# Kernel tuning notes

Measured on AMD Instinct MI355X. Metric: run time of the kernel, lower is better.

## Reference

```python
import jax, jax.numpy as jnp
import numpy as np

D_MODEL = 1024
OUTPUT_DIM = 1024
NUM_HEADS = 16
HEAD_DIM = D_MODEL // NUM_HEADS


def _xavier(key, shape):
    fan_in, fan_out = shape[1], shape[0]
    limit = float(np.sqrt(6.0 / (fan_in + fan_out)))
    return jax.random.uniform(key, shape, jnp.float32, -limit, limit)


def setup_inputs() -> dict:
    key = jax.random.key(0)
    k_h, k_q, k_k, k_o = jax.random.split(key, 4)
    H = jax.random.normal(k_h, (2, 2048, D_MODEL), dtype=jnp.float32)
    # nn.Linear weights are [out, in]; xavier_uniform on weights, default (uniform) biases left as zeros-equivalent
    Wq = _xavier(k_q, (D_MODEL, D_MODEL))
    bq = jnp.zeros((D_MODEL,), jnp.float32)
    Wk = _xavier(k_k, (D_MODEL, D_MODEL))
    bk = jnp.zeros((D_MODEL,), jnp.float32)
    Wo = _xavier(k_o, (OUTPUT_DIM, D_MODEL))
    bo = jnp.zeros((OUTPUT_DIM,), jnp.float32)
    return {"H": H, "Wq": Wq, "bq": bq, "Wk": Wk, "bk": bk, "Wo": Wo, "bo": bo}


def reference(H, Wq, bq, Wk, bk, Wo, bo):
    B, S, _ = H.shape
    Q = H @ Wq.T + bq  # [B,S,D]
    K = H @ Wk.T + bk
    # split heads -> [B,nh,S,hd]
    Qh = Q.reshape(B, S, NUM_HEADS, HEAD_DIM).transpose(0, 2, 1, 3)
    Kh = K.reshape(B, S, NUM_HEADS, HEAD_DIM).transpose(0, 2, 1, 3)
    Vh = H.reshape(B, S, NUM_HEADS, HEAD_DIM).transpose(0, 2, 1, 3)
    scale = 1.0 / jnp.sqrt(jnp.float32(HEAD_DIM))
    A = jnp.einsum('bhqd,bhkd->bhqk', Qh, Kh) * scale  # [B,nh,S,S]
    A = jax.nn.softmax(A, axis=-1)
    out = jnp.einsum('bhqk,bhkd->bhqd', A, Vh)  # [B,nh,S,hd]
    out = out.transpose(0, 2, 1, 3).reshape(B, S, D_MODEL)
    return out @ Wo.T + bo
```

## Files before the change

### kernel.cpp

```cpp
#include <hip/hip_runtime.h>
#include <stdint.h>

#define BB 2
#define SS 2048
#define DD 1024
#define NH 16
#define HD 64
#define MM 4096

typedef __bf16 bf16x8 __attribute__((ext_vector_type(8)));
typedef __bf16 bf16x4 __attribute__((ext_vector_type(4)));
typedef float  f32x4  __attribute__((ext_vector_type(4)));

__device__ __forceinline__ unsigned short f2bf(float f) {
    __bf16 h = (__bf16)f;
    return __builtin_bit_cast(unsigned short, h);
}

__device__ __forceinline__ void async_cp16(const void* g, const void* l) {
    __builtin_amdgcn_global_load_lds(
        (const __attribute__((address_space(1))) void*)(uintptr_t)g,
        (__attribute__((address_space(3))) void*)(uint32_t)(uintptr_t)l,
        16, 0, 0);
}

__device__ __forceinline__ f32x4 mfma16(bf16x8 a, bf16x8 b, f32x4 c) {
    return __builtin_amdgcn_mfma_f32_16x16x32_bf16(a, b, c, 0, 0, 0);
}

__global__ __launch_bounds__(256) void k_prep(const float* __restrict__ H,
                                              const float* __restrict__ Wq,
                                              const float* __restrict__ Wk,
                                              const float* __restrict__ Wo,
                                              unsigned short* __restrict__ Hb,
                                              unsigned short* __restrict__ Vt,
                                              unsigned short* __restrict__ Wqb,
                                              unsigned short* __restrict__ Wkb,
                                              unsigned short* __restrict__ Wob) {
    __shared__ float tile[128][68];
    const int bx = blockIdx.x;
    const int t = threadIdx.x;
    if (bx >= 512) {
        int g = bx - 512;
        const float* src; unsigned short* dst; int base;
        if (g < 512)       { src = Wq; dst = Wqb; base = g; }
        else if (g < 1024) { src = Wk; dst = Wkb; base = g - 512; }
        else               { src = Wo; dst = Wob; base = g - 1024; }
        int i = (base * 256 + t) * 8;
        float4 a = *(const float4*)(src + i);
        float4 b = *(const float4*)(src + i + 4);
        unsigned short o[8];
        o[0] = f2bf(a.x); o[1] = f2bf(a.y); o[2] = f2bf(a.z); o[3] = f2bf(a.w);
        o[4] = f2bf(b.x); o[5] = f2bf(b.y); o[6] = f2bf(b.z); o[7] = f2bf(b.w);
        *(ulonglong2*)(dst + i) = *(ulonglong2*)o;
        return;
    }
    const int sb = bx & 15, h = (bx >> 4) & 15, b = bx >> 8;
    const int col4 = t & 15;
    const int srow0 = t >> 4;
#pragma unroll
    for (int p = 0; p < 8; ++p) {
        int s = p * 16 + srow0;
        float4 v = *(const float4*)(H + (size_t)(b * SS + sb * 128 + s) * DD + h * HD + col4 * 4);
        *(float4*)&tile[s][col4 * 4] = v;
    }
    __syncthreads();
#pragma unroll
    for (int it = 0; it < 4; ++it) {
        int task = it * 256 + t;
        int s = task >> 3;
        int dg = task & 7;
        unsigned short pk[8];
#pragma unroll
        for (int j = 0; j < 8; ++j) pk[j] = f2bf(tile[s][dg * 8 + j]);
        *(ulonglong2*)(Hb + (size_t)(b * SS + sb * 128 + s) * DD + h * HD + dg * 8) = *(ulonglong2*)pk;
    }
#pragma unroll
    for (int it = 0; it < 4; ++it) {
        int task = it * 256 + t;
        int d = task >> 4;
        int sg = task & 15;
        unsigned short pk[8];
#pragma unroll
        for (int j = 0; j < 8; ++j) pk[j] = f2bf(tile[sg * 8 + j][d]);
        *(ulonglong2*)(Vt + (size_t)((b * NH + h) * HD + d) * SS + sb * 128 + sg * 8) = *(ulonglong2*)pk;
    }
}

template <int TM, bool BF16OUT>
__device__ __forceinline__ void gemm_body(const unsigned short* __restrict__ A,
                                          const unsigned short* __restrict__ Bt,
                                          const float* __restrict__ bias,
                                          void* __restrict__ Cp, float oscale) {
    constexpr int MT = TM / 32;
    constexpr int AR = TM / 32;
    __shared__ unsigned short lsA[2][TM * 64];
    __shared__ unsigned short lsB[2][128 * 64];
    const int tid = threadIdx.x;
    const int lane = tid & 63;
    const int w = tid >> 6;
    const int wm = w & 1, wn = w >> 1;
    const int r = lane & 15, quad = lane >> 4;
    const int mBase = blockIdx.y * TM;
    const int nBase = blockIdx.x * 128;

    const unsigned short* gA[AR]; uint laOff[AR];
#pragma unroll
    for (int t = 0; t < AR; ++t) {
        int l = t * 256 + tid;
        int c = l ^ ((l >> 3) & 7);
        int row = c >> 3, kc = c & 7;
        gA[t] = A + (size_t)(mBase + row) * 1024 + kc * 8;
        laOff[t] = l * 8;
    }
    const unsigned short* gB[4]; uint lbOff[4];
#pragma unroll
    for (int t = 0; t < 4; ++t) {
        int l = t * 256 + tid;
        int c = l ^ ((l >> 3) & 7);
        int row = c >> 3, kc = c & 7;
        gB[t] = Bt + (size_t)(nBase + row) * 1024 + kc * 8;
        lbOff[t] = l * 8;
    }
    uint aOff[2][MT], bOff[2][4];
#pragma unroll
    for (int hh = 0; hh < 2; ++hh) {
#pragma unroll
        for (int mt = 0; mt < MT; ++mt) {
            int rowA = wm * (TM / 2) + mt * 16 + r;
            int c = rowA * 8 + hh * 4 + quad;
            aOff[hh][mt] = (uint)((c ^ ((c >> 3) & 7)) * 8);
        }
#pragma unroll
        for (int nt = 0; nt < 4; ++nt) {
            int rowB = wn * 64 + nt * 16 + r;
            int c = rowB * 8 + hh * 4 + quad;
            bOff[hh][nt] = (uint)((c ^ ((c >> 3) & 7)) * 8);
        }
    }

    f32x4 acc[MT][4];
#pragma unroll
    for (int i = 0; i < MT; ++i)
#pragma unroll
        for (int j = 0; j < 4; ++j) acc[i][j] = f32x4{0.f, 0.f, 0.f, 0.f};

    auto stage = [&](int buf) {
#pragma unroll
        for (int t = 0; t < AR; ++t) { async_cp16(gA[t], &lsA[buf][laOff[t]]); gA[t] += 64; }
#pragma unroll
        for (int t = 0; t < 4; ++t)  { async_cp16(gB[t], &lsB[buf][lbOff[t]]); gB[t] += 64; }
    };

    stage(0);
    for (int kb = 0; kb < 16; ++kb) {
        const int cur = kb & 1;
        __syncthreads();
        if (kb + 1 < 16) stage(cur ^ 1);

#pragma unroll
        for (int hh = 0; hh < 2; ++hh) {
            bf16x8 af[MT], bf[4];
#pragma unroll
            for (int mt = 0; mt < MT; ++mt) af[mt] = *(const bf16x8*)&lsA[cur][aOff[hh][mt]];
#pragma unroll
            for (int nt = 0; nt < 4; ++nt)  bf[nt] = *(const bf16x8*)&lsB[cur][bOff[hh][nt]];
#pragma unroll
            for (int mt = 0; mt < MT; ++mt)
#pragma unroll
                for (int nt = 0; nt < 4; ++nt)
                    acc[mt][nt] = mfma16(af[mt], bf[nt], acc[mt][nt]);
        }
    }

    float bv[4];
#pragma unroll
    for (int nt = 0; nt < 4; ++nt) bv[nt] = bias[nBase + wn * 64 + nt * 16 + r];
#pragma unroll
    for (int mt = 0; mt < MT; ++mt)
#pragma unroll
        for (int nt = 0; nt < 4; ++nt) {
            int colg = nBase + wn * 64 + nt * 16 + r;
#pragma unroll
            for (int reg = 0; reg < 4; ++reg) {
                int rowg = mBase + wm * (TM / 2) + mt * 16 + quad * 4 + reg;
                float v = (acc[mt][nt][reg] + bv[nt]) * oscale;
                if (BF16OUT)
                    ((unsigned short*)Cp)[(size_t)rowg * 1024 + colg] = f2bf(v);
                else
                    ((float*)Cp)[(size_t)rowg * 1024 + colg] = v;
            }
        }
}

#define QSCALE 0.1803368801111137f

__global__ __launch_bounds__(256) void k_gemm_qk(const unsigned short* __restrict__ Hb,
                                                 const unsigned short* __restrict__ Wqb,
                                                 const unsigned short* __restrict__ Wkb,
                                                 const float* __restrict__ bq,
                                                 const float* __restrict__ bk,
                                                 unsigned short* __restrict__ Q,
                                                 unsigned short* __restrict__ K) {
    const unsigned short* Bt = blockIdx.z ? Wkb : Wqb;
    const float* bias = blockIdx.z ? bk : bq;
    unsigned short* C = blockIdx.z ? K : Q;
    float os = blockIdx.z ? 1.0f : QSCALE;
    gemm_body<128, true>(Hb, Bt, bias, C, os);
}

__global__ __launch_bounds__(256) void k_gemm_out(const unsigned short* __restrict__ Ctx,
                                                  const unsigned short* __restrict__ Wob,
                                                  const float* __restrict__ bo,
                                                  float* __restrict__ Out) {
    gemm_body<64, false>(Ctx, Wob, bo, Out, 1.0f);
}

__global__ __launch_bounds__(256) void k_attn(const unsigned short* __restrict__ Q,
                                              const unsigned short* __restrict__ K,
                                              const unsigned short* __restrict__ Vt,
                                              unsigned short* __restrict__ Ctx) {
    __shared__ unsigned short lsK[2][128 * 64];
    __shared__ unsigned short lsV[2][128 * 64];
    __shared__ unsigned short lsP[4 * 2048];
    const int tid = threadIdx.x;
    const int lane = tid & 63;
    const int w = tid >> 6;
    const int r = lane & 15, quad = lane >> 4;
    const int id = blockIdx.x;
    const int xcd = id & 7, j = id >> 3;
    const int hb = xcd + 8 * (j & 3);
    const int qb = j >> 2;
    const int h = hb & 15, b = hb >> 4;

    bf16x8 aq[2][2];
#pragma unroll
    for (int sub = 0; sub < 2; ++sub) {
        const int qrow = qb * 128 + w * 32 + sub * 16 + r;
        const size_t qoff = (size_t)(b * SS + qrow) * DD + h * HD;
        aq[sub][0] = *(const bf16x8*)(Q + qoff + quad * 8);
        aq[sub][1] = *(const bf16x8*)(Q + qoff + 32 + quad * 8);
    }

    f32x4 accO[2][4];
#pragma unroll
    for (int sub = 0; sub < 2; ++sub)
#pragma unroll
        for (int nt = 0; nt < 4; ++nt) accO[sub][nt] = f32x4{0.f, 0.f, 0.f, 0.f};
    float lsum[2][4] = {{0.f, 0.f, 0.f, 0.f}, {0.f, 0.f, 0.f, 0.f}};

    const unsigned short* gK[4]; const unsigned short* gV[4]; uint lO[4];
#pragma unroll
    for (int t = 0; t < 4; ++t) {
        int l = t * 256 + tid;
        int c = l ^ ((l >> 3) & 7);
        int half = c >> 9, kc = c & 7;
        int rr = (c >> 3) & 63;
        int srow = half * 64 + 4 * (rr & 15) + (rr >> 4);
        gK[t] = K + (size_t)(b * SS + srow) * DD + h * HD + kc * 8;
        gV[t] = Vt + (size_t)((b * NH + h) * HD + rr) * SS + half * 64 + kc * 8;
        lO[t] = l * 8;
    }
    uint off[2][4];
#pragma unroll
    for (int t = 0; t < 2; ++t)
#pragma unroll
        for (int nt = 0; nt < 4; ++nt) {
            int rowX = nt * 16 + r;
            int c = rowX * 8 + t * 4 + quad;
            off[t][nt] = (uint)((c ^ ((c >> 3) & 7)) * 8);
        }
    uint pw[4], pr[2];
#pragma unroll
    for (int reg = 0; reg < 4; ++reg) {
        int prow = quad * 4 + reg;
        pw[reg] = (uint)(prow * 64 + ((r >> 1) ^ (prow & 7)) * 8 + (r & 1) * 4);
    }
#pragma unroll
    for (int t = 0; t < 2; ++t)
        pr[t] = (uint)(r * 64 + ((4 * t + quad) ^ (r & 7)) * 8);
    unsigned short* Pw = lsP + w * 2048;

    auto stage = [&](int buf) {
#pragma unroll
        for (int t = 0; t < 4; ++t) {
            async_cp16(gK[t], &lsK[buf][lO[t]]); gK[t] += 128 * DD;
            async_cp16(gV[t], &lsV[buf][lO[t]]); gV[t] += 128;
        }
    };

    stage(0);
    for (int kt = 0; kt < 16; ++kt) {
        const int cur = kt & 1;
        __syncthreads();
        if (kt + 1 < 16) stage(cur ^ 1);

#pragma unroll
        for (int half = 0; half < 2; ++half) {
            const uint ho = (uint)half * 4096;

            f32x4 s[2][4];
#pragma unroll
            for (int sub = 0; sub < 2; ++sub)
#pragma unroll
                for (int nt = 0; nt < 4; ++nt) s[sub][nt] = f32x4{0.f, 0.f, 0.f, 0.f};
#pragma unroll
            for (int t = 0; t < 2; ++t)
#pragma unroll
                for (int nt = 0; nt < 4; ++nt) {
                    bf16x8 bk = *(const bf16x8*)&lsK[cur][ho + off[t][nt]];
                    s[0][nt] = mfma16(aq[0][t], bk, s[0][nt]);
                    s[1][nt] = mfma16(aq[1][t], bk, s[1][nt]);
                }

#pragma unroll
            for (int sub = 0; sub < 2; ++sub)
#pragma unroll
                for (int reg = 0; reg < 4; ++reg) {
                    float p0 = __builtin_amdgcn_exp2f(s[sub][0][reg]);
                    float p1 = __builtin_amdgcn_exp2f(s[sub][1][reg]);
                    float p2 = __builtin_amdgcn_exp2f(s[sub][2][reg]);
                    float p3 = __builtin_amdgcn_exp2f(s[sub][3][reg]);
                    lsum[sub][reg] += (p0 + p1) + (p2 + p3);
                    bf16x4 pk = {(__bf16)p0, (__bf16)p1, (__bf16)p2, (__bf16)p3};
                    *(bf16x4*)&Pw[sub * 1024 + pw[reg]] = pk;
                }

#pragma unroll
            for (int t = 0; t < 2; ++t) {
                bf16x8 ap0 = *(const bf16x8*)&Pw[pr[t]];
                bf16x8 ap1 = *(const bf16x8*)&Pw[1024 + pr[t]];
#pragma unroll
                for (int nt = 0; nt < 4; ++nt) {
                    bf16x8 bv = *(const bf16x8*)&lsV[cur][ho + off[t][nt]];
                    accO[0][nt] = mfma16(ap0, bv, accO[0][nt]);
                    accO[1][nt] = mfma16(ap1, bv, accO[1][nt]);
                }
            }
        }
    }

#pragma unroll
    for (int sub = 0; sub < 2; ++sub) {
        float linv[4];
#pragma unroll
        for (int reg = 0; reg < 4; ++reg) {
            float l = lsum[sub][reg];
            l += __shfl_xor(l, 1);
            l += __shfl_xor(l, 2);
            l += __shfl_xor(l, 4);
            l += __shfl_xor(l, 8);
            linv[reg] = 1.0f / l;
        }
#pragma unroll
        for (int nt = 0; nt < 4; ++nt) {
            int d = nt * 16 + r;
#pragma unroll
            for (int reg = 0; reg < 4; ++reg) {
                int qr = qb * 128 + w * 32 + sub * 16 + quad * 4 + reg;
                Ctx[(size_t)(b * SS + qr) * DD + h * HD + d] = f2bf(accO[sub][nt][reg] * linv[reg]);
            }
        }
    }
}

extern "C" void kernel_launch(void* const* d_in, const int* in_sizes, int n_in,
                              void* d_out, int out_size, void* d_ws, size_t ws_size,
                              hipStream_t stream) {
    (void)in_sizes; (void)n_in; (void)out_size; (void)ws_size;
    const float* H  = (const float*)d_in[0];
    const float* Wq = (const float*)d_in[1];
    const float* bq = (const float*)d_in[2];
    const float* Wk = (const float*)d_in[3];
    const float* bk = (const float*)d_in[4];
    const float* Wo = (const float*)d_in[5];
    const float* bo = (const float*)d_in[6];
    float* Out = (float*)d_out;

    char* ws = (char*)d_ws;
    unsigned short* Hb  = (unsigned short*)(ws);
    unsigned short* Qb  = (unsigned short*)(ws + 8388608);
    unsigned short* Kb  = (unsigned short*)(ws + 16777216);
    unsigned short* Ctx = (unsigned short*)(ws + 25165824);
    unsigned short* Vt  = (unsigned short*)(ws + 33554432);
    unsigned short* Wqb = (unsigned short*)(ws + 41943040);
    unsigned short* Wkb = (unsigned short*)(ws + 44040192);
    unsigned short* Wob = (unsigned short*)(ws + 46137344);

    k_prep<<<dim3(2048), dim3(256), 0, stream>>>(H, Wq, Wk, Wo, Hb, Vt, Wqb, Wkb, Wob);
    k_gemm_qk<<<dim3(8, 32, 2), dim3(256), 0, stream>>>(Hb, Wqb, Wkb, bq, bk, Qb, Kb);
    k_attn<<<dim3(512), dim3(256), 0, stream>>>(Qb, Kb, Vt, Ctx);
    k_gemm_out<<<dim3(8, 64, 1), dim3(256), 0, stream>>>(Ctx, Wob, bo, Out);
}
```

Before: 176.8 us.

## Software-pipeline attention PV against next QK tile and remap GEMM block order

The attention loop now uses 64-key tiles, with a triple-buffered V and double-buffered per-wave P. The P·V MFMAs for the previous tile are issued after the QK MFMAs of the current tile, so exp/softmax work and matrix work can overlap. The GEMM kernels switch to a 1D grid with explicit tile mapping that groups blocks by column tile for better L2 reuse. This costs more shared memory and more loop iterations with barriers.

Result: faster. 169.6 us (-4.1%).

```diff
diff --git a/kernel.cpp b/kernel.cpp
--- a/kernel.cpp
+++ b/kernel.cpp
@@ -91,7 +91,8 @@
 __device__ __forceinline__ void gemm_body(const unsigned short* __restrict__ A,
                                           const unsigned short* __restrict__ Bt,
                                           const float* __restrict__ bias,
-                                          void* __restrict__ Cp, float oscale) {
+                                          void* __restrict__ Cp, float oscale,
+                                          int mBase, int nBase) {
     constexpr int MT = TM / 32;
     constexpr int AR = TM / 32;
     __shared__ unsigned short lsA[2][TM * 64];
@@ -101,8 +102,6 @@
     const int w = tid >> 6;
     const int wm = w & 1, wn = w >> 1;
     const int r = lane & 15, quad = lane >> 4;
-    const int mBase = blockIdx.y * TM;
-    const int nBase = blockIdx.x * 128;
 
     const unsigned short* gA[AR]; uint laOff[AR];
 #pragma unroll
@@ -202,27 +201,32 @@
                                                  const float* __restrict__ bk,
                                                  unsigned short* __restrict__ Q,
                                                  unsigned short* __restrict__ K) {
-    const unsigned short* Bt = blockIdx.z ? Wkb : Wqb;
-    const float* bias = blockIdx.z ? bk : bq;
-    unsigned short* C = blockIdx.z ? K : Q;
-    float os = blockIdx.z ? 1.0f : QSCALE;
-    gemm_body<128, true>(Hb, Bt, bias, C, os);
+    const int id = blockIdx.x;
+    const int x = id >> 6, yp = id & 63;
+    const int z = yp >> 5, y = yp & 31;
+    const unsigned short* Bt = z ? Wkb : Wqb;
+    const float* bias = z ? bk : bq;
+    unsigned short* C = z ? K : Q;
+    float os = z ? 1.0f : QSCALE;
+    gemm_body<128, true>(Hb, Bt, bias, C, os, y * 128, x * 128);
 }
 
 __global__ __launch_bounds__(256) void k_gemm_out(const unsigned short* __restrict__ Ctx,
                                                   const unsigned short* __restrict__ Wob,
                                                   const float* __restrict__ bo,
                                                   float* __restrict__ Out) {
-    gemm_body<64, false>(Ctx, Wob, bo, Out, 1.0f);
+    const int id = blockIdx.x;
+    const int x = id >> 6, y = id & 63;
+    gemm_body<64, false>(Ctx, Wob, bo, Out, 1.0f, y * 64, x * 128);
 }
 
 __global__ __launch_bounds__(256) void k_attn(const unsigned short* __restrict__ Q,
                                               const unsigned short* __restrict__ K,
                                               const unsigned short* __restrict__ Vt,
                                               unsigned short* __restrict__ Ctx) {
-    __shared__ unsigned short lsK[2][128 * 64];
-    __shared__ unsigned short lsV[2][128 * 64];
-    __shared__ unsigned short lsP[4 * 2048];
+    __shared__ unsigned short lsK[2][64 * 64];
+    __shared__ unsigned short lsV[3][64 * 64];
+    __shared__ unsigned short lsP[4 * 2 * 2048];
     const int tid = threadIdx.x;
     const int lane = tid & 63;
     const int w = tid >> 6;
@@ -249,16 +253,15 @@
         for (int nt = 0; nt < 4; ++nt) accO[sub][nt] = f32x4{0.f, 0.f, 0.f, 0.f};
     float lsum[2][4] = {{0.f, 0.f, 0.f, 0.f}, {0.f, 0.f, 0.f, 0.f}};
 
-    const unsigned short* gK[4]; const unsigned short* gV[4]; uint lO[4];
-#pragma unroll
-    for (int t = 0; t < 4; ++t) {
+    const unsigned short* gK[2]; const unsigned short* gV[2]; uint lO[2];
+#pragma unroll
+    for (int t = 0; t < 2; ++t) {
         int l = t * 256 + tid;
         int c = l ^ ((l >> 3) & 7);
-        int half = c >> 9, kc = c & 7;
-        int rr = (c >> 3) & 63;
-        int srow = half * 64 + 4 * (rr & 15) + (rr >> 4);
+        int row = c >> 3, kc = c & 7;
+        int srow = 4 * (row & 15) + (row >> 4);
         gK[t] = K + (size_t)(b * SS + srow) * DD + h * HD + kc * 8;
-        gV[t] = Vt + (size_t)((b * NH + h) * HD + rr) * SS + half * 64 + kc * 8;
+        gV[t] = Vt + (size_t)((b * NH + h) * HD + row) * SS + kc * 8;
         lO[t] = l * 8;
     }
     uint off[2][4];
@@ -279,63 +282,79 @@
 #pragma unroll
     for (int t = 0; t < 2; ++t)
         pr[t] = (uint)(r * 64 + ((4 * t + quad) ^ (r & 7)) * 8);
-    unsigned short* Pw = lsP + w * 2048;
-
-    auto stage = [&](int buf) {
-#pragma unroll
-        for (int t = 0; t < 4; ++t) {
-            async_cp16(gK[t], &lsK[buf][lO[t]]); gK[t] += 128 * DD;
-            async_cp16(gV[t], &lsV[buf][lO[t]]); gV[t] += 128;
+    unsigned short* Pw = lsP + w * 4096;
+
+    auto stage = [&](int kb, int vb) {
+#pragma unroll
+        for (int t = 0; t < 2; ++t) {
+            async_cp16(gK[t], &lsK[kb][lO[t]]); gK[t] += 64 * DD;
+            async_cp16(gV[t], &lsV[vb][lO[t]]); gV[t] += 64;
         }
     };
 
-    stage(0);
-    for (int kt = 0; kt < 16; ++kt) {
+    stage(0, 0);
+    for (int kt = 0; kt < 32; ++kt) {
         const int cur = kt & 1;
         __syncthreads();
-        if (kt + 1 < 16) stage(cur ^ 1);
-
-#pragma unroll
-        for (int half = 0; half < 2; ++half) {
-            const uint ho = (uint)half * 4096;
-
-            f32x4 s[2][4];
-#pragma unroll
-            for (int sub = 0; sub < 2; ++sub)
-#pragma unroll
-                for (int nt = 0; nt < 4; ++nt) s[sub][nt] = f32x4{0.f, 0.f, 0.f, 0.f};
-#pragma unroll
-            for (int t = 0; t < 2; ++t)
+        if (kt + 1 < 32) stage(cur ^ 1, (kt + 1) % 3);
+
+        f32x4 s[2][4];
+#pragma unroll
+        for (int sub = 0; sub < 2; ++sub)
+#pragma unroll
+            for (int nt = 0; nt < 4; ++nt) s[sub][nt] = f32x4{0.f, 0.f, 0.f, 0.f};
+#pragma unroll
+        for (int t = 0; t < 2; ++t)
+#pragma unroll
+            for (int nt = 0; nt < 4; ++nt) {
+                bf16x8 bk = *(const bf16x8*)&lsK[cur][off[t][nt]];
+                s[0][nt] = mfma16(aq[0][t], bk, s[0][nt]);
+                s[1][nt] = mfma16(aq[1][t], bk, s[1][nt]);
+            }
+
+        if (kt > 0) {
+            const unsigned short* Pp = Pw + (cur ^ 1) * 2048;
+            const unsigned short* Vp = lsV[(kt + 2) % 3];
+#pragma unroll
+            for (int t = 0; t < 2; ++t) {
+                bf16x8 ap0 = *(const bf16x8*)&Pp[pr[t]];
+                bf16x8 ap1 = *(const bf16x8*)&Pp[1024 + pr[t]];
 #pragma unroll
                 for (int nt = 0; nt < 4; ++nt) {
-                    bf16x8 bk = *(const bf16x8*)&lsK[cur][ho + off[t][nt]];
-                    s[0][nt] = mfma16(aq[0][t], bk, s[0][nt]);
-                    s[1][nt] = mfma16(aq[1][t], bk, s[1][nt]);
-                }
-
-#pragma unroll
-            for (int sub = 0; sub < 2; ++sub)
-#pragma unroll
-                for (int reg = 0; reg < 4; ++reg) {
-                    float p0 = __builtin_amdgcn_exp2f(s[sub][0][reg]);
-                    float p1 = __builtin_amdgcn_exp2f(s[sub][1][reg]);
-                    float p2 = __builtin_amdgcn_exp2f(s[sub][2][reg]);
-                    float p3 = __builtin_amdgcn_exp2f(s[sub][3][reg]);
-                    lsum[sub][reg] += (p0 + p1) + (p2 + p3);
-                    bf16x4 pk = {(__bf16)p0, (__bf16)p1, (__bf16)p2, (__bf16)p3};
-                    *(bf16x4*)&Pw[sub * 1024 + pw[reg]] = pk;
-                }
-
-#pragma unroll
-            for (int t = 0; t < 2; ++t) {
-                bf16x8 ap0 = *(const bf16x8*)&Pw[pr[t]];
-                bf16x8 ap1 = *(const bf16x8*)&Pw[1024 + pr[t]];
-#pragma unroll
-                for (int nt = 0; nt < 4; ++nt) {
-                    bf16x8 bv = *(const bf16x8*)&lsV[cur][ho + off[t][nt]];
+                    bf16x8 bv = *(const bf16x8*)&Vp[off[t][nt]];
                     accO[0][nt] = mfma16(ap0, bv, accO[0][nt]);
                     accO[1][nt] = mfma16(ap1, bv, accO[1][nt]);
                 }
+            }
+        }
+
+        unsigned short* Pc = Pw + cur * 2048;
+#pragma unroll
+        for (int sub = 0; sub < 2; ++sub)
+#pragma unroll
+            for (int reg = 0; reg < 4; ++reg) {
+                float p0 = __builtin_amdgcn_exp2f(s[sub][0][reg]);
+                float p1 = __builtin_amdgcn_exp2f(s[sub][1][reg]);
+                float p2 = __builtin_amdgcn_exp2f(s[sub][2][reg]);
+                float p3 = __builtin_amdgcn_exp2f(s[sub][3][reg]);
+                lsum[sub][reg] += (p0 + p1) + (p2 + p3);
+                bf16x4 pk = {(__bf16)p0, (__bf16)p1, (__bf16)p2, (__bf16)p3};
+                *(bf16x4*)&Pc[sub * 1024 + pw[reg]] = pk;
+            }
+    }
+
+    {
+        const unsigned short* Pp = Pw + 2048;
+        const unsigned short* Vp = lsV[1];
+#pragma unroll
+        for (int t = 0; t < 2; ++t) {
+            bf16x8 ap0 = *(const bf16x8*)&Pp[pr[t]];
+            bf16x8 ap1 = *(const bf16x8*)&Pp[1024 + pr[t]];
+#pragma unroll
+            for (int nt = 0; nt < 4; ++nt) {
+                bf16x8 bv = *(const bf16x8*)&Vp[off[t][nt]];
+                accO[0][nt] = mfma16(ap0, bv, accO[0][nt]);
+                accO[1][nt] = mfma16(ap1, bv, accO[1][nt]);
             }
         }
     }
@@ -388,7 +407,7 @@
     unsigned short* Wob = (unsigned short*)(ws + 46137344);
 
     k_prep<<<dim3(2048), dim3(256), 0, stream>>>(H, Wq, Wk, Wo, Hb, Vt, Wqb, Wkb, Wob);
-    k_gemm_qk<<<dim3(8, 32, 2), dim3(256), 0, stream>>>(Hb, Wqb, Wkb, bq, bk, Qb, Kb);
+    k_gemm_qk<<<dim3(512), dim3(256), 0, stream>>>(Hb, Wqb, Wkb, bq, bk, Qb, Kb);
     k_attn<<<dim3(512), dim3(256), 0, stream>>>(Qb, Kb, Vt, Ctx);
-    k_gemm_out<<<dim3(8, 64, 1), dim3(256), 0, stream>>>(Ctx, Wob, bo, Out);
-}
+    k_gemm_out<<<dim3(512), dim3(256), 0, stream>>>(Ctx, Wob, bo, Out);
+}
```
